# Kernel optimization log

Hardware: AMD Instinct MI355X
Metric: run time of the kernel (lower is better)

The kernel has to match this reference:

```python
import jax, jax.numpy as jnp
import numpy as np

B, G, A, C = 128, 16, 8732, 21
THR = 0.5        # overlap_threshold
NEG_POS = 3      # neg_pos_ratio
VAR0, VAR1 = 0.1, 0.2  # loc_variance


def center_to_point(b):
    cxcy, wh = b[:, :2], b[:, 2:]
    return jnp.concatenate([cxcy - wh / 2, cxcy + wh / 2], axis=-1)


def iou_matrix(a, b):
    # a: [G,4], b: [A,4] point coords (x1,y1,x2,y2) -> [G,A]
    tl = jnp.maximum(a[:, None, :2], b[None, :, :2])
    br = jnp.minimum(a[:, None, 2:], b[None, :, 2:])
    wh = jnp.clip(br - tl, 0.0)
    inter = wh[..., 0] * wh[..., 1]
    area_a = (a[:, 2] - a[:, 0]) * (a[:, 3] - a[:, 1])
    area_b = (b[:, 2] - b[:, 0]) * (b[:, 3] - b[:, 1])
    return inter / (area_a[:, None] + area_b[None, :] - inter)


def encode(anchors, gt_pt):
    # anchors [A,4] (cx,cy,w,h); gt_pt [A,4] point coords
    g_cxcy = (gt_pt[:, :2] + gt_pt[:, 2:]) / 2
    g_wh = gt_pt[:, 2:] - gt_pt[:, :2]
    d_cxcy = (g_cxcy - anchors[:, :2]) / (anchors[:, 2:] * VAR0)
    d_wh = jnp.log(g_wh / anchors[:, 2:]) / VAR1
    return jnp.concatenate([d_cxcy, d_wh], axis=-1)


def match(boxes, labels, anchors, anchors_pt):
    # boxes [G,4] point coords, labels [G] int
    iou = iou_matrix(boxes, anchors_pt)           # [G,A]
    anchor_index = jnp.argmax(iou, axis=1)        # best anchor per gt, [G]
    gt_overlap = jnp.max(iou, axis=0)             # best gt overlap per anchor, [A]
    gt_index = jnp.argmax(iou, axis=0)            # best gt per anchor, [A]
    gt_overlap = gt_overlap.at[anchor_index].set(1.0)
    for i in range(G):
        gt_index = gt_index.at[anchor_index[i]].set(i)
    gt_coords = boxes[gt_index]                   # [A,4]
    loc = encode(anchors, gt_coords)              # [A,4]
    conf = labels[gt_index] + 1                   # [A], 0 reserved for background
    conf = jnp.where(gt_overlap < THR, 0, conf)
    return loc, conf


def setup_inputs() -> dict:
    key = jax.random.key(0)
    k1, k2, k3, k4, k5, k6, k7 = jax.random.split(key, 7)
    predict_offset_coords = jax.random.normal(k1, (B, A, 4), jnp.float32)
    predict_confidences = jax.random.normal(k2, (B, A, C), jnp.float32)
    # valid gt boxes: centers in [0.2,0.8], sizes in [0.05,0.3]
    c = jax.random.uniform(k3, (B, G, 2)) * 0.6 + 0.2
    s = jax.random.uniform(k4, (B, G, 2)) * 0.25 + 0.05
    target_boxes = jnp.concatenate([c - s / 2, c + s / 2], axis=-1)
    target_labels = jax.random.randint(k5, (B, G), 0, C - 1).astype(jnp.int32)
    # anchors in center-coord form (cx,cy,w,h), strictly positive w,h
    acx = jax.random.uniform(k6, (A, 2)) * 0.9 + 0.05
    awh = jax.random.uniform(k7, (A, 2)) * 0.25 + 0.05
    anchors = jnp.concatenate([acx, awh], axis=-1)
    return {"predict_offset_coords": predict_offset_coords,
            "predict_confidences": predict_confidences,
            "target_boxes": target_boxes,
            "target_labels": target_labels,
            "anchors": anchors}


def reference(predict_offset_coords, predict_confidences, target_boxes, target_labels, anchors):
    anchors_pt = center_to_point(anchors)
    loc_t, conf_t = jax.vmap(match, in_axes=(0, 0, None, None))(
        target_boxes, target_labels, anchors, anchors_pt)
    # labels are built without grad in the original (fresh tensors)
    loc_t = jax.lax.stop_gradient(loc_t)
    conf_t = jax.lax.stop_gradient(conf_t)

    is_pos = conf_t > 0                            # [B,A]
    # smooth L1 (beta=1), summed over positive anchors
    diff = predict_offset_coords - loc_t
    ad = jnp.abs(diff)
    sl1 = jnp.where(ad < 1.0, 0.5 * diff * diff, ad - 0.5)
    loss_loc = jnp.sum(sl1 * is_pos[..., None])

    num_pos = jnp.sum(is_pos, axis=1, keepdims=True)      # [B,1]
    n_total = jnp.sum(num_pos).astype(jnp.float32)
    num_neg = jnp.minimum(NEG_POS * num_pos, A - 1)        # [B,1]

    logp = jax.nn.log_softmax(predict_confidences, axis=-1)
    nll = -jnp.take_along_axis(logp, conf_t[..., None], axis=-1)[..., 0]  # [B,A]

    # hard-negative mining via double argsort
    aux = jnp.where(is_pos, 0.0, nll)
    order = jnp.argsort(-aux, axis=1)
    rank = jnp.argsort(order, axis=1)
    is_neg = rank < num_neg

    sel = jnp.logical_or(is_pos, is_neg)
    loss_cls = jnp.sum(jnp.where(sel, nll, 0.0))
    return loss_loc / n_total, loss_cls / n_total
```

## Files before the change

kernel.cpp:

```cpp
#include <hip/hip_runtime.h>
#include <math.h>

#define B_ 128
#define G_ 16
#define A_ 8732
#define C_ 21
#define THR_ 0.5f
#define NEG_POS_ 3
#define VAR0_ 0.1f
#define VAR1_ 0.2f

#define BA_     (B_ * A_)
#define NBLKL_  (BA_ / 256)
#define PCH_    ((NBLKL_ + B_ - 1) / B_)

struct Accum { float loss_loc; float loss_cls; int n_total; int done; };

__global__ __launch_bounds__(512) void k_match(
    const float* __restrict__ tboxes,
    const int*   __restrict__ tlabels,
    const float* __restrict__ anchors,
    int*         __restrict__ match,
    int*         __restrict__ num_pos,
    Accum*                    acc)
{
    const int b    = blockIdx.x;
    const int tid  = threadIdx.x;
    const int lane = tid & 63;
    const int w    = tid >> 6;

    if (b == 0 && tid == 0) {
        acc->loss_loc = 0.f;
        acc->loss_cls = 0.f;
        acc->n_total  = 0;
        acc->done     = 0;
    }

    __shared__ float         s_ov[A_];
    __shared__ unsigned char s_gi[A_];
    __shared__ float s_boxlds[G_ * 4];
    __shared__ int   s_lab[G_];
    __shared__ unsigned long long s_gb[8 * G_];
    __shared__ int   s_forced[G_];
    __shared__ int   s_cnt[8];

    if (tid < G_ * 4) s_boxlds[tid] = tboxes[b * G_ * 4 + tid];
    if (tid < G_)     s_lab[tid]    = tlabels[b * G_ + tid];
    __syncthreads();

    float bx0[G_], by0[G_], bx1[G_], by1[G_], bar[G_];
    #pragma unroll
    for (int g = 0; g < G_; ++g) {
        bx0[g] = s_boxlds[g * 4 + 0];
        by0[g] = s_boxlds[g * 4 + 1];
        bx1[g] = s_boxlds[g * 4 + 2];
        by1[g] = s_boxlds[g * 4 + 3];
        bar[g] = (bx1[g] - bx0[g]) * (by1[g] - by0[g]);
    }

    unsigned long long gb[G_];
    #pragma unroll
    for (int g = 0; g < G_; ++g) gb[g] = 0ull;

    for (int a = tid; a < A_; a += 512) {
        float4 an = ((const float4*)anchors)[a];
        float ax0 = an.x - an.z * 0.5f, ay0 = an.y - an.w * 0.5f;
        float ax1 = an.x + an.z * 0.5f, ay1 = an.y + an.w * 0.5f;
        float area_b = (ax1 - ax0) * (ay1 - ay0);
        float bov = -1.f; int bg = 0;
        #pragma unroll
        for (int g = 0; g < G_; ++g) {
            float tlx = fmaxf(bx0[g], ax0);
            float tly = fmaxf(by0[g], ay0);
            float brx = fminf(bx1[g], ax1);
            float bry = fminf(by1[g], ay1);
            float wdt = fmaxf(brx - tlx, 0.f);
            float hgt = fmaxf(bry - tly, 0.f);
            float inter = wdt * hgt;
            float iou = inter / (bar[g] + area_b - inter);
            if (iou > bov) { bov = iou; bg = g; }
            unsigned long long pk =
                ((unsigned long long)__float_as_uint(iou) << 32) |
                (unsigned)(~(unsigned)a);
            if (pk > gb[g]) gb[g] = pk;
        }
        s_ov[a] = bov;
        s_gi[a] = (unsigned char)bg;
    }

    #pragma unroll
    for (int g = 0; g < G_; ++g) {
        #pragma unroll
        for (int off = 32; off > 0; off >>= 1) {
            unsigned long long o = __shfl_down(gb[g], off);
            if (o > gb[g]) gb[g] = o;
        }
    }
    if (lane == 0) {
        #pragma unroll
        for (int g = 0; g < G_; ++g) s_gb[w * G_ + g] = gb[g];
    }
    __syncthreads();
    if (tid < G_) {
        unsigned long long m = 0ull;
        #pragma unroll
        for (int wv = 0; wv < 8; ++wv) {
            unsigned long long v = s_gb[wv * G_ + tid];
            if (v > m) m = v;
        }
        s_forced[tid] = (int)(~(unsigned)(m & 0xFFFFFFFFull));
    }
    __syncthreads();
    if (tid == 0) {
        for (int g = 0; g < G_; ++g) {
            int a = s_forced[g];
            s_ov[a] = 1.0f;
            s_gi[a] = (unsigned char)g;
        }
    }
    __syncthreads();

    int cnt = 0;
    for (int a = tid; a < A_; a += 512) {
        float ov = s_ov[a];
        int g = s_gi[a];
        int conf = (ov < THR_) ? 0 : (s_lab[g] + 1);
        match[b * A_ + a] = conf | (g << 8);
        cnt += (conf > 0);
    }
    #pragma unroll
    for (int off = 32; off > 0; off >>= 1) cnt += __shfl_down(cnt, off);
    if (lane == 0) s_cnt[w] = cnt;
    __syncthreads();
    if (tid == 0) {
        int t = 0;
        #pragma unroll
        for (int wv = 0; wv < 8; ++wv) t += s_cnt[wv];
        num_pos[b] = t;
    }
}

__global__ __launch_bounds__(256) void k_loss(
    const float* __restrict__ pred_off,
    const float* __restrict__ pred_conf,
    const float* __restrict__ tboxes,
    const float* __restrict__ anchors,
    const int*   __restrict__ match,
    float*       __restrict__ aux,
    float*       __restrict__ part_loc,
    float*       __restrict__ part_cls)
{
    const int tid  = threadIdx.x;
    const int i    = blockIdx.x * 256 + tid;
    const int lane = tid & 63;
    const int w    = tid >> 6;

    __shared__ float4 s_conf4[(256 * C_) / 4];
    __shared__ float  s_lloc[4];
    __shared__ float  s_pnll[4];

    const float4* g4 = (const float4*)pred_conf + (size_t)blockIdx.x * (256 * C_ / 4);
    #pragma unroll
    for (int k = 0; k < 6; ++k) {
        int idx = tid + k * 256;
        if (idx < 256 * C_ / 4) s_conf4[idx] = g4[idx];
    }
    __syncthreads();

    const float* sc = (const float*)s_conf4 + tid * C_;

    int mk   = match[i];
    int conf = mk & 0xff;
    int g    = mk >> 8;

    float m = sc[0];
    #pragma unroll
    for (int c = 1; c < C_; ++c) m = fmaxf(m, sc[c]);
    float s = 0.f;
    #pragma unroll
    for (int c = 0; c < C_; ++c) s += __expf(sc[c] - m);
    float lse = m + __logf(s);

    float xc  = sc[conf];
    float nll = lse - xc;
    bool  pos = conf > 0;

    float lloc = 0.f, pnll = 0.f;
    aux[i] = pos ? 0.f : nll;

    if (pos) {
        pnll = nll;
        int b = i / A_;
        int a = i - b * A_;
        float4 an = ((const float4*)anchors)[a];
        float4 bx = ((const float4*)tboxes)[b * G_ + g];
        float gcx = (bx.x + bx.z) * 0.5f, gcy = (bx.y + bx.w) * 0.5f;
        float gw = bx.z - bx.x, gh = bx.w - bx.y;
        float l0 = (gcx - an.x) / (an.z * VAR0_);
        float l1 = (gcy - an.y) / (an.w * VAR0_);
        float l2 = logf(gw / an.z) / VAR1_;
        float l3 = logf(gh / an.w) / VAR1_;
        float4 p = ((const float4*)pred_off)[i];
        float d, ad;
        d = p.x - l0; ad = fabsf(d); lloc += (ad < 1.f) ? 0.5f * d * d : ad - 0.5f;
        d = p.y - l1; ad = fabsf(d); lloc += (ad < 1.f) ? 0.5f * d * d : ad - 0.5f;
        d = p.z - l2; ad = fabsf(d); lloc += (ad < 1.f) ? 0.5f * d * d : ad - 0.5f;
        d = p.w - l3; ad = fabsf(d); lloc += (ad < 1.f) ? 0.5f * d * d : ad - 0.5f;
    }

    #pragma unroll
    for (int off = 32; off > 0; off >>= 1) {
        lloc += __shfl_down(lloc, off);
        pnll += __shfl_down(pnll, off);
    }
    if (lane == 0) { s_lloc[w] = lloc; s_pnll[w] = pnll; }
    __syncthreads();
    if (tid == 0) {
        part_loc[blockIdx.x] = s_lloc[0] + s_lloc[1] + s_lloc[2] + s_lloc[3];
        part_cls[blockIdx.x] = s_pnll[0] + s_pnll[1] + s_pnll[2] + s_pnll[3];
    }
}

#define NPT_ 35
__global__ __launch_bounds__(256) void k_select(
    const float* __restrict__ aux,
    const int*   __restrict__ num_pos,
    const float* __restrict__ part_loc,
    const float* __restrict__ part_cls,
    Accum*                    acc,
    float*       __restrict__ out)
{
    const int b    = blockIdx.x;
    const int tid  = threadIdx.x;
    const int lane = tid & 63;
    const int w    = tid >> 6;

    __shared__ int   s_c[2][4];
    __shared__ int   s_cf[4];
    __shared__ float s_sf[4];
    __shared__ float s_pl, s_pc;

    {
        float L = 0.f, P = 0.f;
        int base = b * PCH_;
        if (tid < PCH_) {
            int idx = base + tid;
            if (idx < NBLKL_) { L = part_loc[idx]; P = part_cls[idx]; }
        }
        #pragma unroll
        for (int off = 32; off > 0; off >>= 1) {
            L += __shfl_down(L, off);
            P += __shfl_down(P, off);
        }
        if (tid == 0) { s_pl = L; s_pc = P; }
    }

    unsigned u[NPT_];
    #pragma unroll
    for (int j = 0; j < NPT_; ++j) {
        int a = tid + j * 256;
        u[j] = (a < A_) ? __float_as_uint(aux[(size_t)b * A_ + a]) : 0u;
    }

    const int npos = num_pos[b];
    const int K = min(NEG_POS_ * npos, A_ - 1);

    unsigned lo = 0u, hi = 0x7f800000u;
    int it = 0;
    while (lo < hi) {
        unsigned mid = (lo + hi) >> 1;
        int c = 0;
        #pragma unroll
        for (int j = 0; j < NPT_; ++j) c += (u[j] > mid);
        #pragma unroll
        for (int off = 32; off > 0; off >>= 1) c += __shfl_down(c, off);
        if (lane == 0) s_c[it & 1][w] = c;
        __syncthreads();
        int total = s_c[it & 1][0] + s_c[it & 1][1] + s_c[it & 1][2] + s_c[it & 1][3];
        if (total >= K) lo = mid + 1; else hi = mid;
        ++it;
    }

    int c = 0; float sm = 0.f;
    #pragma unroll
    for (int j = 0; j < NPT_; ++j) {
        if (u[j] > lo) { c++; sm += __uint_as_float(u[j]); }
    }
    #pragma unroll
    for (int off = 32; off > 0; off >>= 1) {
        c  += __shfl_down(c, off);
        sm += __shfl_down(sm, off);
    }
    if (lane == 0) { s_cf[w] = c; s_sf[w] = sm; }
    __syncthreads();

    if (tid == 0) {
        int   ct = s_cf[0] + s_cf[1] + s_cf[2] + s_cf[3];
        float st = s_sf[0] + s_sf[1] + s_sf[2] + s_sf[3];
        float T  = __uint_as_float(lo);

        atomicAdd(&acc->loss_loc, s_pl);
        atomicAdd(&acc->loss_cls, s_pc + st + (float)(K - ct) * T);
        atomicAdd(&acc->n_total,  npos);
        __threadfence();
        int old = atomicAdd(&acc->done, 1);
        if (old == B_ - 1) {
            __threadfence();
            float lloc = atomicAdd(&acc->loss_loc, 0.f);
            float lcls = atomicAdd(&acc->loss_cls, 0.f);
            float n    = (float)atomicAdd(&acc->n_total, 0);
            out[0] = lloc / n;
            out[1] = lcls / n;
        }
    }
}

extern "C" void kernel_launch(void* const* d_in, const int* in_sizes, int n_in,
                              void* d_out, int out_size, void* d_ws, size_t ws_size,
                              hipStream_t stream) {
    const float* pred_off  = (const float*)d_in[0];
    const float* pred_conf = (const float*)d_in[1];
    const float* tboxes    = (const float*)d_in[2];
    const int*   tlabels   = (const int*)  d_in[3];
    const float* anchors   = (const float*)d_in[4];
    float* out = (float*)d_out;

    char* ws = (char*)d_ws;
    int*   match_ws = (int*)ws;     ws += (size_t)BA_ * sizeof(int);
    float* aux_ws   = (float*)ws;   ws += (size_t)BA_ * sizeof(float);
    float* ploc_ws  = (float*)ws;   ws += (size_t)((NBLKL_ + 3) & ~3) * sizeof(float);
    float* pcls_ws  = (float*)ws;   ws += (size_t)((NBLKL_ + 3) & ~3) * sizeof(float);
    int*   npos_ws  = (int*)ws;     ws += (size_t)((B_ + 3) & ~3) * sizeof(int);
    Accum* acc      = (Accum*)ws;

    k_match<<<B_, 512, 0, stream>>>(tboxes, tlabels, anchors, match_ws, npos_ws, acc);
    k_loss<<<NBLKL_, 256, 0, stream>>>(pred_off, pred_conf, tboxes, anchors,
                                       match_ws, aux_ws, ploc_ws, pcls_ws);
    k_select<<<B_, 256, 0, stream>>>(aux_ws, npos_ws, ploc_ws, pcls_ws, acc, out);
}
```

Baseline: 226.6 us.

## Fuse loss and hard-negative selection kernels via last-blocks atomic handoff

Merges the per-anchor loss kernel and the per-batch selection kernel into one launch. Each block takes a ticket from an atomic counter, and the last B blocks to finish spin-wait until every block has arrived, then run the selection for one batch row each. This removes one kernel launch and the gap between kernels. In exchange the tail blocks busy-wait, the selection blocks now carry the larger shared-memory and register footprint of both stages, and a second counter is needed for the final reduction.

```diff
diff --git a/kernel.cpp b/kernel.cpp
--- a/kernel.cpp
+++ b/kernel.cpp
@@ -13,8 +13,9 @@
 #define BA_     (B_ * A_)
 #define NBLKL_  (BA_ / 256)
 #define PCH_    ((NBLKL_ + B_ - 1) / B_)
-
-struct Accum { float loss_loc; float loss_cls; int n_total; int done; };
+#define NPT_    35
+
+struct Accum { float loss_loc; float loss_cls; int n_total; int done; int done2; int pad[3]; };
 
 __global__ __launch_bounds__(512) void k_match(
     const float* __restrict__ tboxes,
@@ -34,6 +35,7 @@
         acc->loss_cls = 0.f;
         acc->n_total  = 0;
         acc->done     = 0;
+        acc->done2    = 0;
     }
 
     __shared__ float         s_ov[A_];
@@ -140,15 +142,18 @@
     }
 }
 
-__global__ __launch_bounds__(256) void k_loss(
+__global__ __launch_bounds__(256) void k_loss_sel(
     const float* __restrict__ pred_off,
     const float* __restrict__ pred_conf,
     const float* __restrict__ tboxes,
     const float* __restrict__ anchors,
     const int*   __restrict__ match,
+    const int*   __restrict__ num_pos,
     float*       __restrict__ aux,
     float*       __restrict__ part_loc,
-    float*       __restrict__ part_cls)
+    float*       __restrict__ part_cls,
+    Accum*                    acc,
+    float*       __restrict__ out)
 {
     const int tid  = threadIdx.x;
     const int i    = blockIdx.x * 256 + tid;
@@ -158,6 +163,11 @@
     __shared__ float4 s_conf4[(256 * C_) / 4];
     __shared__ float  s_lloc[4];
     __shared__ float  s_pnll[4];
+    __shared__ int    s_c[2][4];
+    __shared__ int    s_cf[4];
+    __shared__ float  s_sf[4];
+    __shared__ float  s_pl, s_pc;
+    __shared__ int    s_old;
 
     const float4* g4 = (const float4*)pred_conf + (size_t)blockIdx.x * (256 * C_ / 4);
     #pragma unroll
@@ -219,26 +229,22 @@
         part_loc[blockIdx.x] = s_lloc[0] + s_lloc[1] + s_lloc[2] + s_lloc[3];
         part_cls[blockIdx.x] = s_pnll[0] + s_pnll[1] + s_pnll[2] + s_pnll[3];
     }
-}
-
-#define NPT_ 35
-__global__ __launch_bounds__(256) void k_select(
-    const float* __restrict__ aux,
-    const int*   __restrict__ num_pos,
-    const float* __restrict__ part_loc,
-    const float* __restrict__ part_cls,
-    Accum*                    acc,
-    float*       __restrict__ out)
-{
-    const int b    = blockIdx.x;
-    const int tid  = threadIdx.x;
-    const int lane = tid & 63;
-    const int w    = tid >> 6;
-
-    __shared__ int   s_c[2][4];
-    __shared__ int   s_cf[4];
-    __shared__ float s_sf[4];
-    __shared__ float s_pl, s_pc;
+
+    __threadfence();
+    __syncthreads();
+    if (tid == 0) s_old = atomicAdd(&acc->done, 1);
+    __syncthreads();
+    const int old = s_old;
+    if (old < NBLKL_ - B_) return;
+
+    const int b = old - (NBLKL_ - B_);
+    if (b >= B_) return;
+
+    if (tid == 0) {
+        while (atomicAdd(&acc->done, 0) < NBLKL_) __builtin_amdgcn_s_sleep(10);
+    }
+    __syncthreads();
+    __threadfence();
 
     {
         float L = 0.f, P = 0.f;
@@ -303,14 +309,14 @@
         atomicAdd(&acc->loss_cls, s_pc + st + (float)(K - ct) * T);
         atomicAdd(&acc->n_total,  npos);
         __threadfence();
-        int old = atomicAdd(&acc->done, 1);
-        if (old == B_ - 1) {
+        int o2 = atomicAdd(&acc->done2, 1);
+        if (o2 == B_ - 1) {
             __threadfence();
-            float lloc = atomicAdd(&acc->loss_loc, 0.f);
-            float lcls = atomicAdd(&acc->loss_cls, 0.f);
-            float n    = (float)atomicAdd(&acc->n_total, 0);
-            out[0] = lloc / n;
-            out[1] = lcls / n;
+            float llocT = atomicAdd(&acc->loss_loc, 0.f);
+            float lclsT = atomicAdd(&acc->loss_cls, 0.f);
+            float n     = (float)atomicAdd(&acc->n_total, 0);
+            out[0] = llocT / n;
+            out[1] = lclsT / n;
         }
     }
 }
@@ -334,7 +340,7 @@
     Accum* acc      = (Accum*)ws;
 
     k_match<<<B_, 512, 0, stream>>>(tboxes, tlabels, anchors, match_ws, npos_ws, acc);
-    k_loss<<<NBLKL_, 256, 0, stream>>>(pred_off, pred_conf, tboxes, anchors,
-                                       match_ws, aux_ws, ploc_ws, pcls_ws);
-    k_select<<<B_, 256, 0, stream>>>(aux_ws, npos_ws, ploc_ws, pcls_ws, acc, out);
+    k_loss_sel<<<NBLKL_, 256, 0, stream>>>(pred_off, pred_conf, tboxes, anchors,
+                                           match_ws, npos_ws, aux_ws,
+                                           ploc_ws, pcls_ws, acc, out);
 }
```

Result: slower. 597.0 us (+163.5%).
